# Kernel tuning notes

Hardware: AMD Instinct MI355X
Metric: run time of the kernel (lower is better)

Reference implementation:

```python
import jax, jax.numpy as jnp
import numpy as np

TAU = 0.07
MARGIN = 0.2
NUM_SPECIES = 64  # matches fill_max of species_ids


def _l2norm(x):
    return x / jnp.linalg.norm(x, axis=-1, keepdims=True)


def setup_inputs() -> dict:
    key = jax.random.key(0)
    k1, k2, k3 = jax.random.split(key, 3)
    B, D = 8192, 256
    species_embed = _l2norm(jax.random.normal(k1, (B, D), dtype=jnp.float32))
    text_embed = _l2norm(jax.random.normal(k2, (B, D), dtype=jnp.float32))
    species_ids = jax.random.randint(k3, (B,), 0, NUM_SPECIES, dtype=jnp.int32)
    return {"species_embed": species_embed, "text_embed": text_embed,
            "species_ids": species_ids}


def reference(species_embed, text_embed, species_ids):
    B = species_embed.shape[0]
    dtype = species_embed.dtype

    sim = species_embed @ text_embed.T                      # (B, B)
    same = species_ids[:, None] == species_ids[None, :]     # (B, B) bool, symmetric
    diag_sim = jnp.diagonal(sim)                            # (B,)

    # ---- intra-species symmetric InfoNCE (per-species CE, averaged over species)
    logits = sim / TAU
    neg_inf = jnp.finfo(dtype).min
    masked = jnp.where(same, logits, neg_inf)               # restrict to same-species cols
    diag_logit = diag_sim / TAU
    ce_v2t = jax.scipy.special.logsumexp(masked, axis=1) - diag_logit   # per-row CE
    ce_t2v = jax.scipy.special.logsumexp(masked.T, axis=1) - diag_logit # transpose: same mask is symmetric

    ones = jnp.ones((B,), dtype=dtype)
    counts = jax.ops.segment_sum(ones, species_ids, num_segments=NUM_SPECIES)          # group sizes
    seg_v2t = jax.ops.segment_sum(ce_v2t, species_ids, num_segments=NUM_SPECIES)
    seg_t2v = jax.ops.segment_sum(ce_t2v, species_ids, num_segments=NUM_SPECIES)
    valid_s = counts >= 2                                   # groups with <2 members skipped
    per_species = (seg_v2t + seg_t2v) / (2.0 * jnp.maximum(counts, 1.0))
    n_valid = jnp.maximum(jnp.sum(valid_s.astype(dtype)), 1.0)
    loss_infonce = jnp.sum(jnp.where(valid_s, per_species, 0.0)) / n_valid

    # ---- cross-species triplet (pos = mean same-species sim excl. self, neg = mean diff-species sim)
    same_f = same.astype(dtype)
    row_same_sum = jnp.sum(sim * same_f, axis=1)            # includes diagonal
    row_sum = jnp.sum(sim, axis=1)
    pos_cnt = jnp.sum(same_f, axis=1) - 1.0
    neg_cnt = B - jnp.sum(same_f, axis=1)
    pos_mean = (row_same_sum - diag_sim) / jnp.maximum(pos_cnt, 1.0)
    neg_mean = (row_sum - row_same_sum) / jnp.maximum(neg_cnt, 1.0)
    tri = jax.nn.relu(neg_mean - pos_mean + MARGIN)
    valid_i = (pos_cnt > 0) & (neg_cnt > 0)
    n_valid_i = jnp.maximum(jnp.sum(valid_i.astype(dtype)), 1.0)
    loss_triplet = jnp.sum(jnp.where(valid_i, tri, 0.0)) / n_valid_i

    return loss_infonce + loss_triplet
```

## Files before the change

### kernel.cpp

```cpp
#include <hip/hip_runtime.h>
#include <hip/hip_fp16.h>

#define TAU 0.07f
#define MARGIN 0.2f
#define NSPEC 64
#define BB 8192
#define DD 256

#define WS_SCALARS   0
#define WS_COUNTS    288
#define WS_OFFSETS   544
#define WS_LSEROW    1024
#define WS_LSECOL    33792
#define WS_TS        66560
#define WS_T         132096
#define WS_MEMBER    133120
#define ZERO_F4      8256

typedef _Float16 half8 __attribute__((ext_vector_type(8)));
typedef float float4v __attribute__((ext_vector_type(4)));
typedef unsigned int uint4v __attribute__((ext_vector_type(4)));

__device__ __forceinline__ uint4v pack8(float4 a, float4 b) {
  half8 h;
  h[0] = (_Float16)a.x; h[1] = (_Float16)a.y; h[2] = (_Float16)a.z; h[3] = (_Float16)a.w;
  h[4] = (_Float16)b.x; h[5] = (_Float16)b.y; h[6] = (_Float16)b.z; h[7] = (_Float16)b.w;
  return __builtin_bit_cast(uint4v, h);
}

__global__ void k1_all(const int* __restrict__ ids, int* counts_g, int* offsets_g,
                       int* memberList, float* scalars, float4v* zb) {
  __shared__ int cnt[NSPEC];
  __shared__ int off[NSPEC];
  int tid = threadIdx.x;
  float4v z4 = {0.f, 0.f, 0.f, 0.f};
  for (int u = tid; u < ZERO_F4; u += 1024) zb[u] = z4;
  if (tid < 8) ((unsigned*)scalars)[tid] = 0u;
  if (tid < NSPEC) cnt[tid] = 0;
  __syncthreads();
  int myS[8], myP[8];
  #pragma unroll
  for (int r = 0; r < 8; ++r) {
    int i = r * 1024 + tid;
    int s = ids[i];
    myS[r] = s;
    myP[r] = atomicAdd(&cnt[s], 1);
  }
  __syncthreads();
  if (tid < NSPEC) {
    int o = 0;
    for (int t = 0; t < NSPEC; ++t) o += (t < tid) ? cnt[t] : 0;
    off[tid] = o;
    offsets_g[tid] = o;
    int c = cnt[tid];
    counts_g[tid] = c;
    unsigned long long bv = __ballot(c >= 2);
    float nvi = (c >= 2 && c <= BB - 1) ? (float)c : 0.f;
    for (int o2 = 1; o2 < 64; o2 <<= 1) nvi += __shfl_xor(nvi, o2);
    if (tid == 0) {
      scalars[2] = (float)__popcll(bv);
      scalars[3] = nvi;
    }
  }
  __syncthreads();
  #pragma unroll
  for (int r = 0; r < 8; ++r) {
    int i = r * 1024 + tid;
    memberList[off[myS[r]] + myP[r]] = i;
  }
}

__global__ void k2_ts(const float* __restrict__ tx, const int* __restrict__ counts,
                      const int* __restrict__ offsets, const int* __restrict__ memberList,
                      float* Ts) {
  int s = blockIdx.x, r = blockIdx.y;
  int m = counts[s], g0 = offsets[s];
  int k0 = (m * r) >> 3, k1 = (m * (r + 1)) >> 3;
  if (k0 >= k1) return;
  int d = threadIdx.x;
  float acc = 0.f;
  for (int k = k0; k < k1; ++k) acc += tx[memberList[g0 + k] * DD + d];
  atomicAdd(&Ts[s * DD + d], acc);
}

__global__ void k5_lse(const float* __restrict__ sp, const float* __restrict__ tx,
                       const int* __restrict__ counts, const int* __restrict__ offsets,
                       const int* __restrict__ memberList,
                       const float* __restrict__ Ts, float* T,
                       float* lseRow, float* lseCol) {
  if (blockIdx.x == 0 && blockIdx.y == 3 && blockIdx.z == 1) {
    int d = threadIdx.x;
    float acc = 0.f;
    #pragma unroll
    for (int s = 0; s < NSPEC; ++s) acc += Ts[s * DD + d];
    T[d] = acc;
  }

  __shared__ uint4v lds5[1536];
  int s = blockIdx.x;
  int m = counts[s];
  int g0 = offsets[s];
  int tid = threadIdx.x;
  int lane = tid & 63, wv = tid >> 6;
  int quad = lane >> 4, cl = lane & 15;

  for (int rt = blockIdx.y; rt * 64 < m; rt += gridDim.y) {
    for (int ct = blockIdx.z; ct * 128 < m; ct += gridDim.z) {
      float4v acc[8];
      #pragma unroll
      for (int cf = 0; cf < 8; ++cf) acc[cf] = (float4v){0.f, 0.f, 0.f, 0.f};

      for (int kc = 0; kc < 4; ++kc) {
        __syncthreads();
        #pragma unroll
        for (int p = 0; p < 6; ++p) {
          int u = p * 256 + tid;
          int isB = u >= 512;
          int v = isB ? (u - 512) : u;
          int row = v >> 3;
          int sub = v & 7;
          int ksl = sub >> 2, q = sub & 3;
          int d0 = kc * 64 + ksl * 32 + q * 8;
          int idx = isB ? (ct * 128 + row) : (rt * 64 + row);
          uint4v val = (uint4v){0u, 0u, 0u, 0u};
          if (idx < m) {
            const float* src = (isB ? tx : sp) + memberList[g0 + idx] * DD + d0;
            float4 f0 = *reinterpret_cast<const float4*>(src);
            float4 f1 = *reinterpret_cast<const float4*>(src + 4);
            val = pack8(f0, f1);
          }
          int dst = isB ? (512 + (ksl * 128 + row) * 4 + q)
                        : ((ksl * 64 + row) * 4 + q);
          lds5[dst] = val;
        }
        __syncthreads();
        #pragma unroll
        for (int ksl = 0; ksl < 2; ++ksl) {
          half8 a = __builtin_bit_cast(half8, lds5[(ksl * 64 + wv * 16 + cl) * 4 + quad]);
          #pragma unroll
          for (int cf = 0; cf < 8; ++cf) {
            half8 b = __builtin_bit_cast(half8, lds5[512 + (ksl * 128 + cf * 16 + cl) * 4 + quad]);
            acc[cf] = __builtin_amdgcn_mfma_f32_16x16x32_f16(a, b, acc[cf], 0, 0, 0);
          }
        }
      }

      int riBase = rt * 64 + wv * 16 + quad * 4;
      float rowAcc[4] = {0.f, 0.f, 0.f, 0.f};
      #pragma unroll
      for (int cf = 0; cf < 8; ++cf) {
        int ci = ct * 128 + cf * 16 + cl;
        bool cv = ci < m;
        float colAcc = 0.f;
        #pragma unroll
        for (int reg = 0; reg < 4; ++reg) {
          bool rv = (riBase + reg) < m;
          float e = (rv && cv) ? __expf(acc[cf][reg] * (1.f / TAU)) : 0.f;
          rowAcc[reg] += e;
          colAcc += e;
        }
        colAcc += __shfl_xor(colAcc, 16);
        colAcc += __shfl_xor(colAcc, 32);
        if (quad == 0 && cv) atomicAdd(&lseCol[g0 + ci], colAcc);
      }
      #pragma unroll
      for (int reg = 0; reg < 4; ++reg) {
        float v = rowAcc[reg];
        v += __shfl_xor(v, 1);
        v += __shfl_xor(v, 2);
        v += __shfl_xor(v, 4);
        v += __shfl_xor(v, 8);
        if (cl == 0 && (riBase + reg) < m) atomicAdd(&lseRow[g0 + riBase + reg], v);
      }
    }
  }
}

__global__ void k6_fused(const float* __restrict__ sp, const float* __restrict__ tx,
                         const int* __restrict__ ids, const int* __restrict__ counts,
                         const int* __restrict__ memberList,
                         const float* __restrict__ Ts, const float* __restrict__ T,
                         const float* __restrict__ lseRow, const float* __restrict__ lseCol,
                         float* scalars, float* out) {
  __shared__ float red[32];
  int tid = threadIdx.x;
  int gt = blockIdx.x * 1024 + tid;
  int g = gt >> 6, lane = gt & 63;
  int i = memberList[g];
  int s = ids[i];
  int m = counts[s];
  float4 a = *reinterpret_cast<const float4*>(sp + i * DD + lane * 4);
  float4 b = *reinterpret_cast<const float4*>(tx + i * DD + lane * 4);
  float4 c = *reinterpret_cast<const float4*>(Ts + s * DD + lane * 4);
  float4 tv = *reinterpret_cast<const float4*>(T + lane * 4);
  float dDiag = a.x * b.x + a.y * b.y + a.z * b.z + a.w * b.w;
  float dTs   = a.x * c.x + a.y * c.y + a.z * c.z + a.w * c.w;
  float dT    = a.x * tv.x + a.y * tv.y + a.z * tv.z + a.w * tv.w;
  #pragma unroll
  for (int o = 1; o < 64; o <<= 1) {
    dDiag += __shfl_xor(dDiag, o);
    dTs   += __shfl_xor(dTs, o);
    dT    += __shfl_xor(dT, o);
  }
  if (lane == 0) {
    float term = 0.f, tri = 0.f;
    if (m >= 2) {
      term = (__logf(lseRow[g]) + __logf(lseCol[g]) - 2.f * dDiag * (1.f / TAU)) /
             (2.f * (float)m);
      float posMean = (dTs - dDiag) / fmaxf((float)(m - 1), 1.f);
      float negMean = (dT - dTs) / fmaxf((float)(BB - m), 1.f);
      if (m <= BB - 1) tri = fmaxf(negMean - posMean + MARGIN, 0.f);
    }
    int wv = tid >> 6;
    red[wv] = term;
    red[16 + wv] = tri;
  }
  __syncthreads();
  if (tid == 0) {
    float infoS = 0.f, triS = 0.f;
    #pragma unroll
    for (int w = 0; w < 16; ++w) { infoS += red[w]; triS += red[16 + w]; }
    atomicAdd(&scalars[1], infoS);
    atomicAdd(&scalars[0], triS);
    __threadfence();
    unsigned prev = atomicAdd((unsigned*)&scalars[4], 1u);
    if (prev == gridDim.x - 1) {
      float fi = atomicAdd(&scalars[1], 0.f);
      float ft = atomicAdd(&scalars[0], 0.f);
      float nv = scalars[2];
      float nvi = scalars[3];
      out[0] = fi / fmaxf(nv, 1.f) + ft / fmaxf(nvi, 1.f);
    }
  }
}

extern "C" void kernel_launch(void* const* d_in, const int* in_sizes, int n_in,
                              void* d_out, int out_size, void* d_ws, size_t ws_size,
                              hipStream_t stream) {
  const float* sp = (const float*)d_in[0];
  const float* tx = (const float*)d_in[1];
  const int* ids = (const int*)d_in[2];
  float* out = (float*)d_out;

  char* ws = (char*)d_ws;
  float* scalars = (float*)(ws + WS_SCALARS);
  int* counts = (int*)(ws + WS_COUNTS);
  int* offsets = (int*)(ws + WS_OFFSETS);
  float* lseRow = (float*)(ws + WS_LSEROW);
  float* lseCol = (float*)(ws + WS_LSECOL);
  float* Ts = (float*)(ws + WS_TS);
  float* T = (float*)(ws + WS_T);
  int* memberList = (int*)(ws + WS_MEMBER);

  k1_all<<<1, 1024, 0, stream>>>(ids, counts, offsets, memberList, scalars,
                                 (float4v*)(ws + WS_LSEROW));
  k2_ts<<<dim3(NSPEC, 8), 256, 0, stream>>>(tx, counts, offsets, memberList, Ts);
  k5_lse<<<dim3(NSPEC, 4, 2), 256, 0, stream>>>(sp, tx, counts, offsets, memberList,
                                                Ts, T, lseRow, lseCol);
  k6_fused<<<BB / 16, 1024, 0, stream>>>(sp, tx, ids, counts, memberList, Ts, T,
                                         lseRow, lseCol, scalars, out);
}
```

Before: 119.5 us.

## Fuse all stages into one cooperative kernel with grid-wide syncs

Replaces four separate kernel launches with a single cooperative kernel of 512 blocks that uses grid.sync between phases: parallel histogram and zeroing, member list build, per-species text sums plus masked MFMA logsumexp tiles, then the final per-sample reduction. The species histogram and member list construction now run across many blocks instead of one, and the global text sum T is accumulated with atomics. This removes launch gaps and the serial single-block setup, at the cost of grid barrier overhead and the occupancy constraints of cooperative launch.

```diff
diff --git a/kernel.cpp b/kernel.cpp
--- a/kernel.cpp
+++ b/kernel.cpp
@@ -1,5 +1,8 @@
 #include <hip/hip_runtime.h>
 #include <hip/hip_fp16.h>
+#include <hip/hip_cooperative_groups.h>
+
+namespace cg = cooperative_groups;
 
 #define TAU 0.07f
 #define MARGIN 0.2f
@@ -8,14 +11,15 @@
 #define DD 256
 
 #define WS_SCALARS   0
-#define WS_COUNTS    288
-#define WS_OFFSETS   544
-#define WS_LSEROW    1024
-#define WS_LSECOL    33792
-#define WS_TS        66560
-#define WS_T         132096
-#define WS_MEMBER    133120
-#define ZERO_F4      8256
+#define WS_CNT2      64
+#define WS_COUNTS    320
+#define WS_OFFSETS   576
+#define WS_HIST8     832
+#define WS_T         3072
+#define WS_LSEROW    4096
+#define WS_LSECOL    36864
+#define WS_TS        68608
+#define WS_MEMBER    134144
 
 typedef _Float16 half8 __attribute__((ext_vector_type(8)));
 typedef float float4v __attribute__((ext_vector_type(4)));
@@ -28,208 +32,226 @@
   return __builtin_bit_cast(uint4v, h);
 }
 
-__global__ void k1_all(const int* __restrict__ ids, int* counts_g, int* offsets_g,
-                       int* memberList, float* scalars, float4v* zb) {
-  __shared__ int cnt[NSPEC];
-  __shared__ int off[NSPEC];
-  int tid = threadIdx.x;
-  float4v z4 = {0.f, 0.f, 0.f, 0.f};
-  for (int u = tid; u < ZERO_F4; u += 1024) zb[u] = z4;
-  if (tid < 8) ((unsigned*)scalars)[tid] = 0u;
-  if (tid < NSPEC) cnt[tid] = 0;
-  __syncthreads();
-  int myS[8], myP[8];
-  #pragma unroll
-  for (int r = 0; r < 8; ++r) {
-    int i = r * 1024 + tid;
+__device__ __forceinline__ float dot4(float4 a, float4 b) {
+  return a.x * b.x + a.y * b.y + a.z * b.z + a.w * b.w;
+}
+
+__global__ void __launch_bounds__(256, 2)
+fused_all(const float* __restrict__ sp, const float* __restrict__ tx,
+          const int* __restrict__ ids, char* __restrict__ ws, float* __restrict__ out) {
+  float* scalars = (float*)(ws + WS_SCALARS);
+  int* cnt2 = (int*)(ws + WS_CNT2);
+  int* counts = (int*)(ws + WS_COUNTS);
+  int* offsets = (int*)(ws + WS_OFFSETS);
+  int* hist8 = (int*)(ws + WS_HIST8);
+  float* T = (float*)(ws + WS_T);
+  float* lseRow = (float*)(ws + WS_LSEROW);
+  float* lseCol = (float*)(ws + WS_LSECOL);
+  float* Ts = (float*)(ws + WS_TS);
+  int* memberList = (int*)(ws + WS_MEMBER);
+
+  cg::grid_group grid = cg::this_grid();
+  int bid = blockIdx.x, tid = threadIdx.x;
+
+  __shared__ union {
+    int lhist[NSPEC];
+    struct { int cnts[NSPEC]; int offs[NSPEC]; } p1;
+    uint4v lds5[1536];
+    float red[8];
+  } sm;
+
+  if (bid < 8) {
+    if (tid < NSPEC) sm.lhist[tid] = 0;
+    __syncthreads();
+    #pragma unroll
+    for (int r = 0; r < 4; ++r) {
+      int i = bid * 1024 + r * 256 + tid;
+      atomicAdd(&sm.lhist[ids[i]], 1);
+    }
+    __syncthreads();
+    if (tid < NSPEC) hist8[bid * NSPEC + tid] = sm.lhist[tid];
+  } else {
+    int z = (bid - 8) * 256 + tid;
+    float4v z4 = {0.f, 0.f, 0.f, 0.f};
+    if (z < 8192) *(float4v*)(ws + WS_T + z * 16) = z4;
+    else if (z < 8212) *(float4v*)(ws + (z - 8192) * 16) = z4;
+  }
+  grid.sync();
+
+  if (bid < 32) {
+    if (tid < NSPEC) {
+      int c = 0;
+      #pragma unroll
+      for (int b = 0; b < 8; ++b) c += hist8[b * NSPEC + tid];
+      sm.p1.cnts[tid] = c;
+    }
+    __syncthreads();
+    if (tid == 0) {
+      int o = 0;
+      for (int s2 = 0; s2 < NSPEC; ++s2) { sm.p1.offs[s2] = o; o += sm.p1.cnts[s2]; }
+    }
+    __syncthreads();
+    int i = bid * 256 + tid;
     int s = ids[i];
-    myS[r] = s;
-    myP[r] = atomicAdd(&cnt[s], 1);
-  }
-  __syncthreads();
-  if (tid < NSPEC) {
-    int o = 0;
-    for (int t = 0; t < NSPEC; ++t) o += (t < tid) ? cnt[t] : 0;
-    off[tid] = o;
-    offsets_g[tid] = o;
-    int c = cnt[tid];
-    counts_g[tid] = c;
-    unsigned long long bv = __ballot(c >= 2);
-    float nvi = (c >= 2 && c <= BB - 1) ? (float)c : 0.f;
-    for (int o2 = 1; o2 < 64; o2 <<= 1) nvi += __shfl_xor(nvi, o2);
-    if (tid == 0) {
-      scalars[2] = (float)__popcll(bv);
-      scalars[3] = nvi;
-    }
-  }
-  __syncthreads();
-  #pragma unroll
-  for (int r = 0; r < 8; ++r) {
-    int i = r * 1024 + tid;
-    memberList[off[myS[r]] + myP[r]] = i;
-  }
-}
-
-__global__ void k2_ts(const float* __restrict__ tx, const int* __restrict__ counts,
-                      const int* __restrict__ offsets, const int* __restrict__ memberList,
-                      float* Ts) {
-  int s = blockIdx.x, r = blockIdx.y;
-  int m = counts[s], g0 = offsets[s];
-  int k0 = (m * r) >> 3, k1 = (m * (r + 1)) >> 3;
-  if (k0 >= k1) return;
-  int d = threadIdx.x;
-  float acc = 0.f;
-  for (int k = k0; k < k1; ++k) acc += tx[memberList[g0 + k] * DD + d];
-  atomicAdd(&Ts[s * DD + d], acc);
-}
-
-__global__ void k5_lse(const float* __restrict__ sp, const float* __restrict__ tx,
-                       const int* __restrict__ counts, const int* __restrict__ offsets,
-                       const int* __restrict__ memberList,
-                       const float* __restrict__ Ts, float* T,
-                       float* lseRow, float* lseCol) {
-  if (blockIdx.x == 0 && blockIdx.y == 3 && blockIdx.z == 1) {
-    int d = threadIdx.x;
-    float acc = 0.f;
-    #pragma unroll
-    for (int s = 0; s < NSPEC; ++s) acc += Ts[s * DD + d];
-    T[d] = acc;
-  }
-
-  __shared__ uint4v lds5[1536];
-  int s = blockIdx.x;
-  int m = counts[s];
-  int g0 = offsets[s];
-  int tid = threadIdx.x;
-  int lane = tid & 63, wv = tid >> 6;
-  int quad = lane >> 4, cl = lane & 15;
-
-  for (int rt = blockIdx.y; rt * 64 < m; rt += gridDim.y) {
-    for (int ct = blockIdx.z; ct * 128 < m; ct += gridDim.z) {
-      float4v acc[8];
-      #pragma unroll
-      for (int cf = 0; cf < 8; ++cf) acc[cf] = (float4v){0.f, 0.f, 0.f, 0.f};
-
-      for (int kc = 0; kc < 4; ++kc) {
-        __syncthreads();
+    int pos = sm.p1.offs[s] + atomicAdd(&cnt2[s], 1);
+    memberList[pos] = i;
+    if (bid == 0) {
+      if (tid < NSPEC) { counts[tid] = sm.p1.cnts[tid]; offsets[tid] = sm.p1.offs[tid]; }
+      if (tid == 0) {
+        float nv = 0.f, nvi = 0.f;
+        for (int s2 = 0; s2 < NSPEC; ++s2) {
+          int c = sm.p1.cnts[s2];
+          if (c >= 2) { nv += 1.f; if (c <= BB - 1) nvi += (float)c; }
+        }
+        scalars[2] = nv; scalars[3] = nvi;
+      }
+    }
+  }
+  grid.sync();
+
+  {
+    int s = bid & 63;
+    int m = counts[s];
+    int g0 = offsets[s];
+    int r = bid >> 6;
+
+    {
+      int k0 = (m * r) >> 3, k1e = (m * (r + 1)) >> 3;
+      if (k0 < k1e) {
+        int d = tid;
+        float acc = 0.f;
+        for (int k = k0; k < k1e; ++k) acc += tx[memberList[g0 + k] * DD + d];
+        atomicAdd(&Ts[s * DD + d], acc);
+        atomicAdd(&T[d], acc);
+      }
+    }
+
+    int lane = tid & 63, wv = tid >> 6;
+    int quad = lane >> 4, cl = lane & 15;
+    int rt0 = (bid >> 6) & 3, ct0 = bid >> 8;
+
+    for (int rt = rt0; rt * 64 < m; rt += 4) {
+      for (int ct = ct0; ct * 128 < m; ct += 2) {
+        float4v acc[8];
         #pragma unroll
-        for (int p = 0; p < 6; ++p) {
-          int u = p * 256 + tid;
-          int isB = u >= 512;
-          int v = isB ? (u - 512) : u;
-          int row = v >> 3;
-          int sub = v & 7;
-          int ksl = sub >> 2, q = sub & 3;
-          int d0 = kc * 64 + ksl * 32 + q * 8;
-          int idx = isB ? (ct * 128 + row) : (rt * 64 + row);
-          uint4v val = (uint4v){0u, 0u, 0u, 0u};
-          if (idx < m) {
-            const float* src = (isB ? tx : sp) + memberList[g0 + idx] * DD + d0;
-            float4 f0 = *reinterpret_cast<const float4*>(src);
-            float4 f1 = *reinterpret_cast<const float4*>(src + 4);
-            val = pack8(f0, f1);
+        for (int cf = 0; cf < 8; ++cf) acc[cf] = (float4v){0.f, 0.f, 0.f, 0.f};
+
+        for (int kc = 0; kc < 4; ++kc) {
+          __syncthreads();
+          #pragma unroll
+          for (int p = 0; p < 6; ++p) {
+            int u = p * 256 + tid;
+            int isB = u >= 512;
+            int v = isB ? (u - 512) : u;
+            int row = v >> 3;
+            int sub = v & 7;
+            int ksl = sub >> 2, q = sub & 3;
+            int d0 = kc * 64 + ksl * 32 + q * 8;
+            int idx = isB ? (ct * 128 + row) : (rt * 64 + row);
+            uint4v val = (uint4v){0u, 0u, 0u, 0u};
+            if (idx < m) {
+              const float* src = (isB ? tx : sp) + memberList[g0 + idx] * DD + d0;
+              float4 f0 = *reinterpret_cast<const float4*>(src);
+              float4 f1 = *reinterpret_cast<const float4*>(src + 4);
+              val = pack8(f0, f1);
+            }
+            int dst = isB ? (512 + (ksl * 128 + row) * 4 + q)
+                          : ((ksl * 64 + row) * 4 + q);
+            sm.lds5[dst] = val;
           }
-          int dst = isB ? (512 + (ksl * 128 + row) * 4 + q)
-                        : ((ksl * 64 + row) * 4 + q);
-          lds5[dst] = val;
-        }
-        __syncthreads();
+          __syncthreads();
+          #pragma unroll
+          for (int ksl = 0; ksl < 2; ++ksl) {
+            half8 a = __builtin_bit_cast(half8, sm.lds5[(ksl * 64 + wv * 16 + cl) * 4 + quad]);
+            #pragma unroll
+            for (int cf = 0; cf < 8; ++cf) {
+              half8 b = __builtin_bit_cast(half8, sm.lds5[512 + (ksl * 128 + cf * 16 + cl) * 4 + quad]);
+              acc[cf] = __builtin_amdgcn_mfma_f32_16x16x32_f16(a, b, acc[cf], 0, 0, 0);
+            }
+          }
+        }
+
+        int riBase = rt * 64 + wv * 16 + quad * 4;
+        float rowAcc[4] = {0.f, 0.f, 0.f, 0.f};
         #pragma unroll
-        for (int ksl = 0; ksl < 2; ++ksl) {
-          half8 a = __builtin_bit_cast(half8, lds5[(ksl * 64 + wv * 16 + cl) * 4 + quad]);
+        for (int cf = 0; cf < 8; ++cf) {
+          int ci = ct * 128 + cf * 16 + cl;
+          bool cv = ci < m;
+          float colAcc = 0.f;
           #pragma unroll
-          for (int cf = 0; cf < 8; ++cf) {
-            half8 b = __builtin_bit_cast(half8, lds5[512 + (ksl * 128 + cf * 16 + cl) * 4 + quad]);
-            acc[cf] = __builtin_amdgcn_mfma_f32_16x16x32_f16(a, b, acc[cf], 0, 0, 0);
+          for (int reg = 0; reg < 4; ++reg) {
+            bool rv = (riBase + reg) < m;
+            float e = (rv && cv) ? __expf(acc[cf][reg] * (1.f / TAU)) : 0.f;
+            rowAcc[reg] += e;
+            colAcc += e;
           }
-        }
-      }
-
-      int riBase = rt * 64 + wv * 16 + quad * 4;
-      float rowAcc[4] = {0.f, 0.f, 0.f, 0.f};
-      #pragma unroll
-      for (int cf = 0; cf < 8; ++cf) {
-        int ci = ct * 128 + cf * 16 + cl;
-        bool cv = ci < m;
-        float colAcc = 0.f;
+          colAcc += __shfl_xor(colAcc, 16);
+          colAcc += __shfl_xor(colAcc, 32);
+          if (quad == 0 && cv) atomicAdd(&lseCol[g0 + ci], colAcc);
+        }
         #pragma unroll
         for (int reg = 0; reg < 4; ++reg) {
-          bool rv = (riBase + reg) < m;
-          float e = (rv && cv) ? __expf(acc[cf][reg] * (1.f / TAU)) : 0.f;
-          rowAcc[reg] += e;
-          colAcc += e;
-        }
-        colAcc += __shfl_xor(colAcc, 16);
-        colAcc += __shfl_xor(colAcc, 32);
-        if (quad == 0 && cv) atomicAdd(&lseCol[g0 + ci], colAcc);
-      }
+          float v = rowAcc[reg];
+          v += __shfl_xor(v, 1);
+          v += __shfl_xor(v, 2);
+          v += __shfl_xor(v, 4);
+          v += __shfl_xor(v, 8);
+          if (cl == 0 && (riBase + reg) < m) atomicAdd(&lseRow[g0 + riBase + reg], v);
+        }
+      }
+    }
+  }
+  grid.sync();
+
+  {
+    int wv = tid >> 6, lane = tid & 63;
+    int wg = bid * 4 + wv;
+    float termAcc = 0.f, triAcc = 0.f;
+    #pragma unroll
+    for (int j = 0; j < 4; ++j) {
+      int g = wg + j * 2048;
+      int i = memberList[g];
+      int s = ids[i];
+      int m = counts[s];
+      float4 a = *reinterpret_cast<const float4*>(sp + i * DD + lane * 4);
+      float4 b = *reinterpret_cast<const float4*>(tx + i * DD + lane * 4);
+      float4 c = *reinterpret_cast<const float4*>(Ts + s * DD + lane * 4);
+      float4 tv = *reinterpret_cast<const float4*>(T + lane * 4);
+      float dDiag = dot4(a, b);
+      float dTs = dot4(a, c);
+      float dT = dot4(a, tv);
       #pragma unroll
-      for (int reg = 0; reg < 4; ++reg) {
-        float v = rowAcc[reg];
-        v += __shfl_xor(v, 1);
-        v += __shfl_xor(v, 2);
-        v += __shfl_xor(v, 4);
-        v += __shfl_xor(v, 8);
-        if (cl == 0 && (riBase + reg) < m) atomicAdd(&lseRow[g0 + riBase + reg], v);
-      }
-    }
-  }
-}
-
-__global__ void k6_fused(const float* __restrict__ sp, const float* __restrict__ tx,
-                         const int* __restrict__ ids, const int* __restrict__ counts,
-                         const int* __restrict__ memberList,
-                         const float* __restrict__ Ts, const float* __restrict__ T,
-                         const float* __restrict__ lseRow, const float* __restrict__ lseCol,
-                         float* scalars, float* out) {
-  __shared__ float red[32];
-  int tid = threadIdx.x;
-  int gt = blockIdx.x * 1024 + tid;
-  int g = gt >> 6, lane = gt & 63;
-  int i = memberList[g];
-  int s = ids[i];
-  int m = counts[s];
-  float4 a = *reinterpret_cast<const float4*>(sp + i * DD + lane * 4);
-  float4 b = *reinterpret_cast<const float4*>(tx + i * DD + lane * 4);
-  float4 c = *reinterpret_cast<const float4*>(Ts + s * DD + lane * 4);
-  float4 tv = *reinterpret_cast<const float4*>(T + lane * 4);
-  float dDiag = a.x * b.x + a.y * b.y + a.z * b.z + a.w * b.w;
-  float dTs   = a.x * c.x + a.y * c.y + a.z * c.z + a.w * c.w;
-  float dT    = a.x * tv.x + a.y * tv.y + a.z * tv.z + a.w * tv.w;
-  #pragma unroll
-  for (int o = 1; o < 64; o <<= 1) {
-    dDiag += __shfl_xor(dDiag, o);
-    dTs   += __shfl_xor(dTs, o);
-    dT    += __shfl_xor(dT, o);
-  }
-  if (lane == 0) {
-    float term = 0.f, tri = 0.f;
-    if (m >= 2) {
-      term = (__logf(lseRow[g]) + __logf(lseCol[g]) - 2.f * dDiag * (1.f / TAU)) /
-             (2.f * (float)m);
-      float posMean = (dTs - dDiag) / fmaxf((float)(m - 1), 1.f);
-      float negMean = (dT - dTs) / fmaxf((float)(BB - m), 1.f);
-      if (m <= BB - 1) tri = fmaxf(negMean - posMean + MARGIN, 0.f);
-    }
-    int wv = tid >> 6;
-    red[wv] = term;
-    red[16 + wv] = tri;
-  }
-  __syncthreads();
-  if (tid == 0) {
-    float infoS = 0.f, triS = 0.f;
-    #pragma unroll
-    for (int w = 0; w < 16; ++w) { infoS += red[w]; triS += red[16 + w]; }
-    atomicAdd(&scalars[1], infoS);
-    atomicAdd(&scalars[0], triS);
-    __threadfence();
-    unsigned prev = atomicAdd((unsigned*)&scalars[4], 1u);
-    if (prev == gridDim.x - 1) {
-      float fi = atomicAdd(&scalars[1], 0.f);
-      float ft = atomicAdd(&scalars[0], 0.f);
-      float nv = scalars[2];
-      float nvi = scalars[3];
-      out[0] = fi / fmaxf(nv, 1.f) + ft / fmaxf(nvi, 1.f);
+      for (int o = 1; o < 64; o <<= 1) {
+        dDiag += __shfl_xor(dDiag, o);
+        dTs   += __shfl_xor(dTs, o);
+        dT    += __shfl_xor(dT, o);
+      }
+      if (lane == 0 && m >= 2) {
+        termAcc += (__logf(lseRow[g]) + __logf(lseCol[g]) - 2.f * dDiag * (1.f / TAU)) /
+                   (2.f * (float)m);
+        if (m <= BB - 1) {
+          float posMean = (dTs - dDiag) / fmaxf((float)(m - 1), 1.f);
+          float negMean = (dT - dTs) / fmaxf((float)(BB - m), 1.f);
+          triAcc += fmaxf(negMean - posMean + MARGIN, 0.f);
+        }
+      }
+    }
+    if (lane == 0) { sm.red[wv] = termAcc; sm.red[4 + wv] = triAcc; }
+    __syncthreads();
+    if (tid == 0) {
+      float infoS = sm.red[0] + sm.red[1] + sm.red[2] + sm.red[3];
+      float triS = sm.red[4] + sm.red[5] + sm.red[6] + sm.red[7];
+      atomicAdd(&scalars[1], infoS);
+      atomicAdd(&scalars[0], triS);
+      __threadfence();
+      unsigned prev = atomicAdd((unsigned*)&scalars[4], 1u);
+      if (prev == (unsigned)(gridDim.x - 1)) {
+        float fi = atomicAdd(&scalars[1], 0.f);
+        float ft = atomicAdd(&scalars[0], 0.f);
+        float nv = atomicAdd(&scalars[2], 0.f);
+        float nvi = atomicAdd(&scalars[3], 0.f);
+        out[0] = fi / fmaxf(nv, 1.f) + ft / fmaxf(nvi, 1.f);
+      }
     }
   }
 }
@@ -241,22 +263,8 @@
   const float* tx = (const float*)d_in[1];
   const int* ids = (const int*)d_in[2];
   float* out = (float*)d_out;
-
   char* ws = (char*)d_ws;
-  float* scalars = (float*)(ws + WS_SCALARS);
-  int* counts = (int*)(ws + WS_COUNTS);
-  int* offsets = (int*)(ws + WS_OFFSETS);
-  float* lseRow = (float*)(ws + WS_LSEROW);
-  float* lseCol = (float*)(ws + WS_LSECOL);
-  float* Ts = (float*)(ws + WS_TS);
-  float* T = (float*)(ws + WS_T);
-  int* memberList = (int*)(ws + WS_MEMBER);
-
-  k1_all<<<1, 1024, 0, stream>>>(ids, counts, offsets, memberList, scalars,
-                                 (float4v*)(ws + WS_LSEROW));
-  k2_ts<<<dim3(NSPEC, 8), 256, 0, stream>>>(tx, counts, offsets, memberList, Ts);
-  k5_lse<<<dim3(NSPEC, 4, 2), 256, 0, stream>>>(sp, tx, counts, offsets, memberList,
-                                                Ts, T, lseRow, lseCol);
-  k6_fused<<<BB / 16, 1024, 0, stream>>>(sp, tx, ids, counts, memberList, Ts, T,
-                                         lseRow, lseCol, scalars, out);
-}
+
+  void* args[] = {(void*)&sp, (void*)&tx, (void*)&ids, (void*)&ws, (void*)&out};
+  hipLaunchCooperativeKernel((void*)fused_all, dim3(512), dim3(256), args, 0, stream);
+}
```

New measurement: 288.8 us. +141.6%, slower.

## Merge Ts accumulation into LSE kernel and accumulate T via atomics

Applied to the files above, without the earlier changes.

Folds the per-species text-sum kernel into the LSE kernel as extra blocks, cutting one kernel launch and letting both kinds of work run concurrently. The global text sum T is now built with atomics from each partial sum instead of a separate reduction pass over Ts. Counts and offsets move within the workspace so that zeroing the first 16 words covers the scalar slots. This adds many atomic updates to T, and T now depends on the workspace zeroing done in the first kernel.

```diff
diff --git a/kernel.cpp b/kernel.cpp
--- a/kernel.cpp
+++ b/kernel.cpp
@@ -8,8 +8,8 @@
 #define DD 256
 
 #define WS_SCALARS   0
-#define WS_COUNTS    288
-#define WS_OFFSETS   544
+#define WS_COUNTS    64
+#define WS_OFFSETS   320
 #define WS_LSEROW    1024
 #define WS_LSECOL    33792
 #define WS_TS        66560
@@ -28,14 +28,19 @@
   return __builtin_bit_cast(uint4v, h);
 }
 
+__device__ __forceinline__ float dot4(float4 a, float4 b) {
+  return a.x * b.x + a.y * b.y + a.z * b.z + a.w * b.w;
+}
+
 __global__ void k1_all(const int* __restrict__ ids, int* counts_g, int* offsets_g,
-                       int* memberList, float* scalars, float4v* zb) {
+                       int* memberList, float* scalars, char* ws) {
   __shared__ int cnt[NSPEC];
   __shared__ int off[NSPEC];
   int tid = threadIdx.x;
   float4v z4 = {0.f, 0.f, 0.f, 0.f};
+  float4v* zb = (float4v*)(ws + WS_LSEROW);
   for (int u = tid; u < ZERO_F4; u += 1024) zb[u] = z4;
-  if (tid < 8) ((unsigned*)scalars)[tid] = 0u;
+  if (tid < 16) ((unsigned*)ws)[tid] = 0u;
   if (tid < NSPEC) cnt[tid] = 0;
   __syncthreads();
   int myS[8], myP[8];
@@ -70,42 +75,37 @@
   }
 }
 
-__global__ void k2_ts(const float* __restrict__ tx, const int* __restrict__ counts,
-                      const int* __restrict__ offsets, const int* __restrict__ memberList,
-                      float* Ts) {
-  int s = blockIdx.x, r = blockIdx.y;
-  int m = counts[s], g0 = offsets[s];
-  int k0 = (m * r) >> 3, k1 = (m * (r + 1)) >> 3;
-  if (k0 >= k1) return;
-  int d = threadIdx.x;
-  float acc = 0.f;
-  for (int k = k0; k < k1; ++k) acc += tx[memberList[g0 + k] * DD + d];
-  atomicAdd(&Ts[s * DD + d], acc);
-}
-
-__global__ void k5_lse(const float* __restrict__ sp, const float* __restrict__ tx,
-                       const int* __restrict__ counts, const int* __restrict__ offsets,
-                       const int* __restrict__ memberList,
-                       const float* __restrict__ Ts, float* T,
-                       float* lseRow, float* lseCol) {
-  if (blockIdx.x == 0 && blockIdx.y == 3 && blockIdx.z == 1) {
-    int d = threadIdx.x;
+__global__ void kmid(const float* __restrict__ sp, const float* __restrict__ tx,
+                     const int* __restrict__ counts, const int* __restrict__ offsets,
+                     const int* __restrict__ memberList,
+                     float* Ts, float* T, float* lseRow, float* lseCol) {
+  __shared__ uint4v lds5[1536];
+  int bid = blockIdx.x;
+  int tid = threadIdx.x;
+
+  if (bid >= 512) {
+    int v = bid - 512;
+    int s = v & 63, r = v >> 6;
+    int m = counts[s], g0 = offsets[s];
+    int k0 = (m * r) >> 3, k1e = (m * (r + 1)) >> 3;
+    if (k0 >= k1e) return;
+    int d = tid;
     float acc = 0.f;
-    #pragma unroll
-    for (int s = 0; s < NSPEC; ++s) acc += Ts[s * DD + d];
-    T[d] = acc;
-  }
-
-  __shared__ uint4v lds5[1536];
-  int s = blockIdx.x;
+    for (int k = k0; k < k1e; ++k) acc += tx[memberList[g0 + k] * DD + d];
+    atomicAdd(&Ts[s * DD + d], acc);
+    atomicAdd(&T[d], acc);
+    return;
+  }
+
+  int s = bid & 63;
   int m = counts[s];
   int g0 = offsets[s];
-  int tid = threadIdx.x;
   int lane = tid & 63, wv = tid >> 6;
   int quad = lane >> 4, cl = lane & 15;
-
-  for (int rt = blockIdx.y; rt * 64 < m; rt += gridDim.y) {
-    for (int ct = blockIdx.z; ct * 128 < m; ct += gridDim.z) {
+  int rt0 = (bid >> 6) & 3, ct0 = (bid >> 8) & 1;
+
+  for (int rt = rt0; rt * 64 < m; rt += 4) {
+    for (int ct = ct0; ct * 128 < m; ct += 2) {
       float4v acc[8];
       #pragma unroll
       for (int cf = 0; cf < 8; ++cf) acc[cf] = (float4v){0.f, 0.f, 0.f, 0.f};
@@ -176,12 +176,12 @@
   }
 }
 
-__global__ void k6_fused(const float* __restrict__ sp, const float* __restrict__ tx,
-                         const int* __restrict__ ids, const int* __restrict__ counts,
-                         const int* __restrict__ memberList,
-                         const float* __restrict__ Ts, const float* __restrict__ T,
-                         const float* __restrict__ lseRow, const float* __restrict__ lseCol,
-                         float* scalars, float* out) {
+__global__ void kend(const float* __restrict__ sp, const float* __restrict__ tx,
+                     const int* __restrict__ ids, const int* __restrict__ counts,
+                     const int* __restrict__ memberList,
+                     const float* __restrict__ Ts, const float* __restrict__ T,
+                     const float* __restrict__ lseRow, const float* __restrict__ lseCol,
+                     float* scalars, float* out) {
   __shared__ float red[32];
   int tid = threadIdx.x;
   int gt = blockIdx.x * 1024 + tid;
@@ -193,9 +193,9 @@
   float4 b = *reinterpret_cast<const float4*>(tx + i * DD + lane * 4);
   float4 c = *reinterpret_cast<const float4*>(Ts + s * DD + lane * 4);
   float4 tv = *reinterpret_cast<const float4*>(T + lane * 4);
-  float dDiag = a.x * b.x + a.y * b.y + a.z * b.z + a.w * b.w;
-  float dTs   = a.x * c.x + a.y * c.y + a.z * c.z + a.w * c.w;
-  float dT    = a.x * tv.x + a.y * tv.y + a.z * tv.z + a.w * tv.w;
+  float dDiag = dot4(a, b);
+  float dTs   = dot4(a, c);
+  float dT    = dot4(a, tv);
   #pragma unroll
   for (int o = 1; o < 64; o <<= 1) {
     dDiag += __shfl_xor(dDiag, o);
@@ -224,7 +224,7 @@
     atomicAdd(&scalars[0], triS);
     __threadfence();
     unsigned prev = atomicAdd((unsigned*)&scalars[4], 1u);
-    if (prev == gridDim.x - 1) {
+    if (prev == (unsigned)(gridDim.x - 1)) {
       float fi = atomicAdd(&scalars[1], 0.f);
       float ft = atomicAdd(&scalars[0], 0.f);
       float nv = scalars[2];
@@ -252,11 +252,9 @@
   float* T = (float*)(ws + WS_T);
   int* memberList = (int*)(ws + WS_MEMBER);
 
-  k1_all<<<1, 1024, 0, stream>>>(ids, counts, offsets, memberList, scalars,
-                                 (float4v*)(ws + WS_LSEROW));
-  k2_ts<<<dim3(NSPEC, 8), 256, 0, stream>>>(tx, counts, offsets, memberList, Ts);
-  k5_lse<<<dim3(NSPEC, 4, 2), 256, 0, stream>>>(sp, tx, counts, offsets, memberList,
-                                                Ts, T, lseRow, lseCol);
-  k6_fused<<<BB / 16, 1024, 0, stream>>>(sp, tx, ids, counts, memberList, Ts, T,
-                                         lseRow, lseCol, scalars, out);
-}
+  k1_all<<<1, 1024, 0, stream>>>(ids, counts, offsets, memberList, scalars, ws);
+  kmid<<<1024, 256, 0, stream>>>(sp, tx, counts, offsets, memberList, Ts, T,
+                                 lseRow, lseCol);
+  kend<<<512, 1024, 0, stream>>>(sp, tx, ids, counts, memberList, Ts, T,
+                                 lseRow, lseCol, scalars, out);
+}
```

Result: slower. 122.0 us (+2.1%).
